# Performance work log

Hardware: AMD Instinct MI355X
Metric: run time of the kernel (lower is better)

Reference implementation:

```python
import jax, jax.numpy as jnp
import numpy as np

N_EMBD = 1024
N_HEAD = 16
HEAD_DIM = N_EMBD // N_HEAD
B, T = 4, 1024
EPS = 1e-5


def _linear_params(key, fan_in, fan_out):
    kw, kb = jax.random.split(key)
    bound = 1.0 / np.sqrt(fan_in)
    W = jax.random.uniform(kw, (fan_in, fan_out), minval=-bound, maxval=bound, dtype=jnp.float32)
    b = jax.random.uniform(kb, (fan_out,), minval=-bound, maxval=bound, dtype=jnp.float32)
    return W, b


def setup_inputs() -> dict:
    key = jax.random.key(0)
    ks = jax.random.split(key, 8)
    x = jax.random.normal(ks[0], (B, T, N_EMBD), dtype=jnp.float32)
    Wq, bq = _linear_params(ks[1], N_EMBD, N_EMBD)
    Wk, bk = _linear_params(ks[2], N_EMBD, N_EMBD)
    Wv, bv = _linear_params(ks[3], N_EMBD, N_EMBD)
    Wp, bp = _linear_params(ks[4], N_EMBD, N_EMBD)
    W1, b1 = _linear_params(ks[5], N_EMBD, 4 * N_EMBD)
    W2, b2 = _linear_params(ks[6], 4 * N_EMBD, N_EMBD)
    g1 = jnp.ones((N_EMBD,), jnp.float32); be1 = jnp.zeros((N_EMBD,), jnp.float32)
    g2 = jnp.ones((N_EMBD,), jnp.float32); be2 = jnp.zeros((N_EMBD,), jnp.float32)
    return {"x": x, "Wq": Wq, "bq": bq, "Wk": Wk, "bk": bk, "Wv": Wv, "bv": bv,
            "Wp": Wp, "bp": bp, "W1": W1, "b1": b1, "W2": W2, "b2": b2,
            "g1": g1, "be1": be1, "g2": g2, "be2": be2}


def _layernorm(x, g, b):
    mu = jnp.mean(x, axis=-1, keepdims=True)
    var = jnp.mean(jnp.square(x - mu), axis=-1, keepdims=True)
    return (x - mu) * jax.lax.rsqrt(var + EPS) * g + b


def _attention(x, Wq, bq, Wk, bk, Wv, bv, Wp, bp):
    Bsz, Tt, C = x.shape
    def heads(W, b):
        return (x @ W + b).reshape(Bsz, Tt, N_HEAD, HEAD_DIM).transpose(0, 2, 1, 3)  # [B,H,T,d]
    q, k, v = heads(Wq, bq), heads(Wk, bk), heads(Wv, bv)
    scores = jnp.einsum('bhqd,bhkd->bhqk', q, k) / np.sqrt(HEAD_DIM).astype(np.float32)
    causal = jnp.tril(jnp.ones((Tt, Tt), dtype=bool))
    scores = jnp.where(causal, scores, -jnp.inf)
    attn = jax.nn.softmax(scores, axis=-1)
    out = jnp.einsum('bhqk,bhkd->bhqd', attn, v)  # [B,H,T,d]
    out = out.transpose(0, 2, 1, 3).reshape(Bsz, Tt, C)
    return out @ Wp + bp


def _ff(x, W1, b1, W2, b2):
    h = jax.nn.gelu(x @ W1 + b1, approximate=False)  # torch nn.GELU default = exact erf
    return h @ W2 + b2


def reference(x, Wq, bq, Wk, bk, Wv, bv, Wp, bp, W1, b1, W2, b2, g1, be1, g2, be2):
    x = x + _attention(_layernorm(x, g1, be1), Wq, bq, Wk, bk, Wv, bv, Wp, bp)
    x = x + _ff(_layernorm(x, g2, be2), W1, b1, W2, b2)
    return x
```

## Files before the change

### kernel.cpp

```cpp
#include <hip/hip_runtime.h>
#include <hip/hip_bf16.h>

typedef __attribute__((ext_vector_type(8))) __bf16 bf16x8;
typedef __attribute__((ext_vector_type(4))) float f32x4;
typedef __attribute__((ext_vector_type(4))) unsigned short u16x4;
typedef unsigned short u16;

#define AS3(p) ((__attribute__((address_space(3))) void*)(p))
#define AS1(p) ((const __attribute__((address_space(1))) void*)(p))

__device__ __forceinline__ u16 f2b(float f) {
    __hip_bfloat16 h = __float2bfloat16(f);
    return __builtin_bit_cast(u16, h);
}

__device__ __forceinline__ float gelu_exact(float v) {
    const float z = v * 0.70710678118654752f;
    const float a = fabsf(z);
    const float t = __builtin_amdgcn_rcpf(1.0f + 0.3275911f * a);
    float p = 1.061405429f;
    p = p * t - 1.453152027f;
    p = p * t + 1.421413741f;
    p = p * t - 0.284496736f;
    p = p * t + 0.254829592f;
    p = p * t;
    float erfv = 1.0f - p * __expf(-a * a);
    erfv = copysignf(erfv, z);
    return 0.5f * v * (1.0f + erfv);
}

__global__ __launch_bounds__(256) void transpose_w(
    const float* __restrict__ W, u16* __restrict__ WT, int K, int N)
{
    __shared__ u16 tile[32][33];
    const int tx = threadIdx.x & 31, ty = threadIdx.x >> 5;
    const int n0 = blockIdx.x * 32, k0 = blockIdx.y * 32;
    #pragma unroll
    for (int p = 0; p < 4; ++p)
        tile[ty + p * 8][tx] = f2b(W[(size_t)(k0 + ty + p * 8) * N + n0 + tx]);
    __syncthreads();
    #pragma unroll
    for (int p = 0; p < 4; ++p)
        WT[(size_t)(n0 + ty + p * 8) * K + k0 + tx] = tile[tx][ty + p * 8];
}

__global__ __launch_bounds__(256) void transpose_w3(
    const float* __restrict__ W0, const float* __restrict__ W1,
    const float* __restrict__ W2, u16* __restrict__ WT)
{
    __shared__ u16 tile[32][33];
    const int z = blockIdx.z;
    const float* W = (z == 0) ? W0 : (z == 1) ? W1 : W2;
    u16* dst = WT + (size_t)z * 1024 * 1024;
    const int tx = threadIdx.x & 31, ty = threadIdx.x >> 5;
    const int n0 = blockIdx.x * 32, k0 = blockIdx.y * 32;
    #pragma unroll
    for (int p = 0; p < 4; ++p)
        tile[ty + p * 8][tx] = f2b(W[(size_t)(k0 + ty + p * 8) * 1024 + n0 + tx]);
    __syncthreads();
    #pragma unroll
    for (int p = 0; p < 4; ++p)
        dst[(size_t)(n0 + ty + p * 8) * 1024 + k0 + tx] = tile[tx][ty + p * 8];
}

__global__ __launch_bounds__(256) void ln_bf16(
    const float* __restrict__ xin, const float* __restrict__ gam,
    const float* __restrict__ bet, u16* __restrict__ yout)
{
    __shared__ float red[8];
    const int row = blockIdx.x, tid = threadIdx.x;
    float4 v = ((const float4*)(xin + (size_t)row * 1024))[tid];
    float s = v.x + v.y + v.z + v.w;
    #pragma unroll
    for (int o = 32; o > 0; o >>= 1) s += __shfl_xor(s, o, 64);
    if ((tid & 63) == 0) red[tid >> 6] = s;
    __syncthreads();
    const float mu = (red[0] + red[1] + red[2] + red[3]) * (1.f / 1024.f);
    const float dx = v.x - mu, dy = v.y - mu, dz = v.z - mu, dw = v.w - mu;
    float sq = dx * dx + dy * dy + dz * dz + dw * dw;
    #pragma unroll
    for (int o = 32; o > 0; o >>= 1) sq += __shfl_xor(sq, o, 64);
    if ((tid & 63) == 0) red[4 + (tid >> 6)] = sq;
    __syncthreads();
    const float var = (red[4] + red[5] + red[6] + red[7]) * (1.f / 1024.f);
    const float inv = rsqrtf(var + 1e-5f);
    const float4 G = ((const float4*)gam)[tid];
    const float4 Bt = ((const float4*)bet)[tid];
    u16x4 o;
    o[0] = f2b(dx * inv * G.x + Bt.x);
    o[1] = f2b(dy * inv * G.y + Bt.y);
    o[2] = f2b(dz * inv * G.z + Bt.z);
    o[3] = f2b(dw * inv * G.w + Bt.w);
    ((u16x4*)(yout + (size_t)row * 1024))[tid] = o;
}

__global__ __launch_bounds__(256) void reduce_ln(
    const float* __restrict__ p0, const float* __restrict__ p1,
    const float* __restrict__ bias, const float* __restrict__ resid,
    const float* __restrict__ gam, const float* __restrict__ bet,
    float* __restrict__ xout, u16* __restrict__ yout)
{
    __shared__ float red[8];
    const int row = blockIdx.x, tid = threadIdx.x;
    const size_t off = (size_t)row * 256 + tid;
    float4 a = ((const float4*)p0)[off];
    const float4 b = ((const float4*)p1)[off];
    const float4 r = ((const float4*)resid)[off];
    const float4 bs = ((const float4*)bias)[tid];
    a.x += b.x + r.x + bs.x; a.y += b.y + r.y + bs.y;
    a.z += b.z + r.z + bs.z; a.w += b.w + r.w + bs.w;
    ((float4*)xout)[off] = a;
    float s = a.x + a.y + a.z + a.w;
    #pragma unroll
    for (int o = 32; o > 0; o >>= 1) s += __shfl_xor(s, o, 64);
    if ((tid & 63) == 0) red[tid >> 6] = s;
    __syncthreads();
    const float mu = (red[0] + red[1] + red[2] + red[3]) * (1.f / 1024.f);
    const float dx = a.x - mu, dy = a.y - mu, dz = a.z - mu, dw = a.w - mu;
    float sq = dx * dx + dy * dy + dz * dz + dw * dw;
    #pragma unroll
    for (int o = 32; o > 0; o >>= 1) sq += __shfl_xor(sq, o, 64);
    if ((tid & 63) == 0) red[4 + (tid >> 6)] = sq;
    __syncthreads();
    const float var = (red[4] + red[5] + red[6] + red[7]) * (1.f / 1024.f);
    const float inv = rsqrtf(var + 1e-5f);
    const float4 G = ((const float4*)gam)[tid];
    const float4 Bt = ((const float4*)bet)[tid];
    u16x4 o;
    o[0] = f2b(dx * inv * G.x + Bt.x);
    o[1] = f2b(dy * inv * G.y + Bt.y);
    o[2] = f2b(dz * inv * G.z + Bt.z);
    o[3] = f2b(dw * inv * G.w + Bt.w);
    ((u16x4*)(yout + (size_t)row * 1024))[tid] = o;
}

__global__ __launch_bounds__(256) void reduce_add(
    const float* __restrict__ p0, const float* __restrict__ p1,
    const float* __restrict__ bias, const float* __restrict__ resid,
    float* __restrict__ out)
{
    const size_t i = (size_t)blockIdx.x * 256 + threadIdx.x;
    float4 a = ((const float4*)p0)[i];
    const float4 b = ((const float4*)p1)[i];
    const float4 r = ((const float4*)resid)[i];
    const float4 bs = ((const float4*)bias)[i & 255];
    a.x += b.x + r.x + bs.x; a.y += b.y + r.y + bs.y;
    a.z += b.z + r.z + bs.z; a.w += b.w + r.w + bs.w;
    ((float4*)out)[i] = a;
}

template <int MODE, int BM, int SK>
__global__ __launch_bounds__(256, (BM == 128 ? 3 : 2)) void gemm_bf16(
    const u16* __restrict__ A, const u16* __restrict__ BT,
    const float* __restrict__ b0, const float* __restrict__ b1,
    const float* __restrict__ b2,
    void* __restrict__ outp, int M, int N, int K)
{
    constexpr int WM = BM / 2;
    constexpr int MI = WM / 16;
    constexpr int NI = 4;
    constexpr int AJ = BM / 64;
    constexpr int AELEM = BM * 32;
    constexpr int BELEM = 128 * 32;
    __shared__ u16 Asm[3 * AELEM];
    __shared__ u16 Bsm[3 * BELEM];

    const int tid = threadIdx.x;
    const int lane = tid & 63, wid = tid >> 6;
    const int wm = wid >> 1, wn = wid & 1;
    const int g = lane >> 4, l16 = lane & 15;
    const int sx = (l16 >> 1) & 3;
    const int sslot = (lane & 3) ^ ((lane >> 3) & 3);

    const int nBN = N >> 7;
    const int per = (M / BM) * nBN;
    const int cpx = gridDim.x >> 3;
    const int wg = (blockIdx.x & 7) * cpx + (blockIdx.x >> 3);
    const int skid = (SK > 1) ? (wg / per) : 0;
    const int rem = wg - skid * per;
    const int bm0 = (rem / nBN) * BM, bn0 = (rem % nBN) * 128;
    const int kb = skid * (K / SK);

    f32x4 acc[MI][NI] = {};

    const u16* aBase = A + (size_t)(bm0 + (lane >> 2)) * K + kb + sslot * 8;
    const u16* bBase = BT + (size_t)(bn0 + (lane >> 2)) * K + kb + sslot * 8;

    auto stage = [&](int kt, int buf) {
        u16* adst = Asm + buf * AELEM + lane * 8;
        u16* bdst = Bsm + buf * BELEM + lane * 8;
        #pragma unroll
        for (int j = 0; j < AJ; ++j) {
            const int ia = wid * AJ + j;
            __builtin_amdgcn_global_load_lds(AS1(aBase + (size_t)(ia * 16) * K + kt),
                                             AS3(adst + ia * 512), 16, 0, 0);
        }
        #pragma unroll
        for (int j = 0; j < 2; ++j) {
            const int ib = wid * 2 + j;
            __builtin_amdgcn_global_load_lds(AS1(bBase + (size_t)(ib * 16) * K + kt),
                                             AS3(bdst + ib * 512), 16, 0, 0);
        }
    };

    const int nt = K / (32 * SK);
    stage(0, 0);
    stage(32, 1);
    int cur = 0, pre = 2;

    for (int t = 0; t < nt; ++t) {
        if (t + 1 < nt) {
            if constexpr (BM == 256) asm volatile("s_waitcnt vmcnt(6)" ::: "memory");
            else                     asm volatile("s_waitcnt vmcnt(4)" ::: "memory");
        } else {
            asm volatile("s_waitcnt vmcnt(0)" ::: "memory");
        }
        __builtin_amdgcn_s_barrier();
        __builtin_amdgcn_sched_barrier(0);

        const u16* asrc = Asm + cur * AELEM;
        const u16* bsrc = Bsm + cur * BELEM;
        bf16x8 af[MI], bfr[NI];
        #pragma unroll
        for (int mi = 0; mi < MI; ++mi) {
            const int r = wm * WM + mi * 16 + l16;
            af[mi] = *(const bf16x8*)(asrc + r * 32 + ((g ^ sx) << 3));
        }
        #pragma unroll
        for (int ni = 0; ni < NI; ++ni) {
            const int c = wn * 64 + ni * 16 + l16;
            bfr[ni] = *(const bf16x8*)(bsrc + c * 32 + ((g ^ sx) << 3));
        }
        if (t + 2 < nt) stage((t + 2) * 32, pre);

        #pragma unroll
        for (int mi = 0; mi < MI; ++mi)
            #pragma unroll
            for (int ni = 0; ni < NI; ++ni)
                acc[mi][ni] = __builtin_amdgcn_mfma_f32_16x16x32_bf16(
                    af[mi], bfr[ni], acc[mi][ni], 0, 0, 0);

        pre = cur;
        cur = (cur == 2) ? 0 : cur + 1;
    }

    #pragma unroll
    for (int mi = 0; mi < MI; ++mi) {
        #pragma unroll
        for (int ni = 0; ni < NI; ++ni) {
            #pragma unroll
            for (int j = 0; j < 4; ++j) {
                const int m = bm0 + wm * WM + mi * 16 + g * 4 + j;
                const int n = bn0 + wn * 64 + ni * 16 + l16;
                float v = acc[mi][ni][j];
                if constexpr (MODE == 0) {
                    const float bias = (n < 1024) ? b0[n]
                                      : (n < 2048) ? b1[n - 1024] : b2[n - 2048];
                    ((u16*)outp)[(size_t)m * N + n] = f2b(v + bias);
                } else if constexpr (MODE == 2) {
                    ((u16*)outp)[(size_t)m * N + n] = f2b(gelu_exact(v + b0[n]));
                } else {
                    float* pout = (float*)outp + (size_t)skid * M * N;
                    pout[(size_t)m * N + n] = v;
                }
            }
        }
    }
}

__global__ __launch_bounds__(256) void attn_fwd(
    const u16* __restrict__ qkv, u16* __restrict__ outp)
{
    __shared__ u16 Ksm[64 * 72];
    __shared__ u16 Vsm[64 * 72];
    __shared__ u16 Psm[4][16 * 72];
    const int tid = threadIdx.x, lane = tid & 63, w = tid >> 6;
    const int lin = blockIdx.y * 8 + blockIdx.x;
    const int xq = (lin >> 3) & 7;
    const int bh = (((lin >> 6) & 7) << 3) | (lin & 7);
    const int b = bh >> 4, h = bh & 15;
    const int g = lane >> 4, l16 = lane & 15;
    const int skv = tid >> 4;
    const int sd4 = (tid & 15) * 4;

    const u16* kvb = qkv + (size_t)(b * 1024) * 3072 + 1024 + h * 64;

    u16x4 kreg[4], vreg[4];
    auto issue = [&](int kv0) {
        const u16* kb = kvb + (size_t)kv0 * 3072;
        #pragma unroll
        for (int i = 0; i < 4; ++i)
            kreg[i] = *(const u16x4*)(kb + (size_t)(skv + 16 * i) * 3072 + sd4);
        #pragma unroll
        for (int i = 0; i < 4; ++i)
            vreg[i] = *(const u16x4*)(kb + (size_t)(4 * skv + i) * 3072 + 1024 + sd4);
    };

    #pragma unroll
    for (int half = 0; half < 2; ++half) {
        const int qt = half ? (15 - xq) : xq;
        const int q0 = qt * 64;

        bf16x8 qf0, qf1;
        {
            const u16* qp = qkv + (size_t)(b * 1024 + q0 + w * 16 + l16) * 3072
                            + h * 64 + g * 8;
            qf0 = *(const bf16x8*)qp;
            qf1 = *(const bf16x8*)(qp + 32);
        }
        float m_run[4] = {-1e30f, -1e30f, -1e30f, -1e30f};
        float l_run[4] = {0.f, 0.f, 0.f, 0.f};
        f32x4 oacc[4] = {};

        issue(0);

        for (int kvt = 0; kvt <= qt; ++kvt) {
            const int kv0 = kvt * 64;
            __syncthreads();
            #pragma unroll
            for (int i = 0; i < 4; ++i)
                *(u16x4*)(Ksm + (skv + 16 * i) * 72 + sd4) = kreg[i];
            #pragma unroll
            for (int j = 0; j < 4; ++j) {
                u16x4 t;
                t[0] = vreg[0][j]; t[1] = vreg[1][j];
                t[2] = vreg[2][j]; t[3] = vreg[3][j];
                *(u16x4*)(Vsm + (sd4 + j) * 72 + 4 * skv) = t;
            }
            __syncthreads();
            if (kvt < qt) issue(kv0 + 64);

            f32x4 s[4];
            #pragma unroll
            for (int t = 0; t < 4; ++t) {
                const bf16x8 kf0 = *(const bf16x8*)(Ksm + (t * 16 + l16) * 72 + g * 8);
                const bf16x8 kf1 = *(const bf16x8*)(Ksm + (t * 16 + l16) * 72 + 32 + g * 8);
                f32x4 z = {};
                z = __builtin_amdgcn_mfma_f32_16x16x32_bf16(qf0, kf0, z, 0, 0, 0);
                z = __builtin_amdgcn_mfma_f32_16x16x32_bf16(qf1, kf1, z, 0, 0, 0);
                s[t] = z;
            }
            float mx[4] = {-1e30f, -1e30f, -1e30f, -1e30f};
            #pragma unroll
            for (int t = 0; t < 4; ++t)
                #pragma unroll
                for (int j = 0; j < 4; ++j) {
                    const int qrow = q0 + w * 16 + g * 4 + j;
                    const int kvc = kv0 + t * 16 + l16;
                    float v = s[t][j] * 0.125f;
                    if (kvc > qrow) v = -1e30f;
                    s[t][j] = v;
                    mx[j] = fmaxf(mx[j], v);
                }
            #pragma unroll
            for (int o = 1; o < 16; o <<= 1)
                #pragma unroll
                for (int j = 0; j < 4; ++j)
                    mx[j] = fmaxf(mx[j], __shfl_xor(mx[j], o, 16));
            float alpha[4], rs[4];
            #pragma unroll
            for (int j = 0; j < 4; ++j) {
                const float mn = fmaxf(m_run[j], mx[j]);
                alpha[j] = __expf(m_run[j] - mn);
                m_run[j] = mn;
                rs[j] = 0.f;
            }
            #pragma unroll
            for (int t = 0; t < 4; ++t)
                #pragma unroll
                for (int j = 0; j < 4; ++j) {
                    const float p = __expf(s[t][j] - m_run[j]);
                    s[t][j] = p;
                    rs[j] += p;
                }
            #pragma unroll
            for (int o = 1; o < 16; o <<= 1)
                #pragma unroll
                for (int j = 0; j < 4; ++j)
                    rs[j] += __shfl_xor(rs[j], o, 16);
            #pragma unroll
            for (int j = 0; j < 4; ++j)
                l_run[j] = l_run[j] * alpha[j] + rs[j];
            #pragma unroll
            for (int dt = 0; dt < 4; ++dt)
                #pragma unroll
                for (int j = 0; j < 4; ++j)
                    oacc[dt][j] *= alpha[j];
            #pragma unroll
            for (int t = 0; t < 4; ++t)
                #pragma unroll
                for (int j = 0; j < 4; ++j)
                    Psm[w][(g * 4 + j) * 72 + t * 16 + l16] = f2b(s[t][j]);
            const bf16x8 pf0 = *(const bf16x8*)(&Psm[w][l16 * 72 + g * 8]);
            const bf16x8 pf1 = *(const bf16x8*)(&Psm[w][l16 * 72 + 32 + g * 8]);
            #pragma unroll
            for (int dt = 0; dt < 4; ++dt) {
                const bf16x8 vf0 = *(const bf16x8*)(Vsm + (dt * 16 + l16) * 72 + g * 8);
                const bf16x8 vf1 = *(const bf16x8*)(Vsm + (dt * 16 + l16) * 72 + 32 + g * 8);
                oacc[dt] = __builtin_amdgcn_mfma_f32_16x16x32_bf16(pf0, vf0, oacc[dt], 0, 0, 0);
                oacc[dt] = __builtin_amdgcn_mfma_f32_16x16x32_bf16(pf1, vf1, oacc[dt], 0, 0, 0);
            }
        }
        #pragma unroll
        for (int dt = 0; dt < 4; ++dt)
            #pragma unroll
            for (int j = 0; j < 4; ++j) {
                const int m = b * 1024 + q0 + w * 16 + g * 4 + j;
                const int col = h * 64 + dt * 16 + l16;
                outp[(size_t)m * 1024 + col] = f2b(oacc[dt][j] / l_run[j]);
            }
    }
}

extern "C" void kernel_launch(void* const* d_in, const int* in_sizes, int n_in,
                              void* d_out, int out_size, void* d_ws, size_t ws_size,
                              hipStream_t stream)
{
    const float* x   = (const float*)d_in[0];
    const float* Wq  = (const float*)d_in[1];
    const float* bq  = (const float*)d_in[2];
    const float* Wk  = (const float*)d_in[3];
    const float* bk  = (const float*)d_in[4];
    const float* Wv  = (const float*)d_in[5];
    const float* bv  = (const float*)d_in[6];
    const float* Wp  = (const float*)d_in[7];
    const float* bp  = (const float*)d_in[8];
    const float* W1  = (const float*)d_in[9];
    const float* b1  = (const float*)d_in[10];
    const float* W2  = (const float*)d_in[11];
    const float* b2  = (const float*)d_in[12];
    const float* g1  = (const float*)d_in[13];
    const float* be1 = (const float*)d_in[14];
    const float* g2  = (const float*)d_in[15];
    const float* be2 = (const float*)d_in[16];

    char* ws = (char*)d_ws;
    const size_t MB = 1024 * 1024;
    u16*   ln_buf = (u16*)(ws);
    u16*   qkv    = (u16*)(ws + 8 * MB);
    u16*   attn_o = (u16*)(ws + 32 * MB);
    float* x1     = (float*)(ws + 40 * MB);
    u16*   hbuf   = (u16*)(ws + 56 * MB);
    u16*   wqkvT  = (u16*)(ws + 88 * MB);
    u16*   wpT    = (u16*)(ws + 94 * MB);
    u16*   w1T    = (u16*)(ws + 96 * MB);
    u16*   w2T    = (u16*)(ws + 104 * MB);
    float* projP  = (float*)(ws + 56 * MB);
    float* ff2P   = (float*)(ws + 8 * MB);

    transpose_w3<<<dim3(32, 32, 3), 256, 0, stream>>>(Wq, Wk, Wv, wqkvT);
    transpose_w<<<dim3(32, 32), 256, 0, stream>>>(Wp, wpT, 1024, 1024);
    transpose_w<<<dim3(128, 32), 256, 0, stream>>>(W1, w1T, 1024, 4096);
    transpose_w<<<dim3(32, 128), 256, 0, stream>>>(W2, w2T, 4096, 1024);

    ln_bf16<<<4096, 256, 0, stream>>>(x, g1, be1, ln_buf);
    gemm_bf16<0, 128, 1><<<768, 256, 0, stream>>>(
        ln_buf, wqkvT, bq, bk, bv, qkv, 4096, 3072, 1024);
    attn_fwd<<<dim3(8, 64), 256, 0, stream>>>(qkv, attn_o);
    gemm_bf16<3, 128, 2><<<512, 256, 0, stream>>>(
        attn_o, wpT, nullptr, nullptr, nullptr, projP, 4096, 1024, 1024);
    reduce_ln<<<4096, 256, 0, stream>>>(
        projP, projP + 4096 * 1024, bp, x, g2, be2, x1, ln_buf);
    gemm_bf16<2, 256, 1><<<512, 256, 0, stream>>>(
        ln_buf, w1T, b1, nullptr, nullptr, hbuf, 4096, 4096, 1024);
    gemm_bf16<3, 128, 2><<<512, 256, 0, stream>>>(
        hbuf, w2T, nullptr, nullptr, nullptr, ff2P, 4096, 1024, 4096);
    reduce_add<<<4096, 256, 0, stream>>>(
        ff2P, ff2P + 4096 * 1024, b2, x1, (float*)d_out);
}
```

Baseline: 221.4 us.

## Double-buffer attention K/V in LDS with XOR swizzle, prescaled Q and exp2

Restructures the flash-attention kernel so K/V tiles are double-buffered in shared memory, with one barrier per iteration instead of two. Padded shared-memory rows are replaced by an XOR swizzle. Q is prescaled by log2(e)/sqrt(d) in the QKV GEMM epilogue so the softmax can use exp2 directly. The causal mask is applied only on the diagonal tile, row sums come from an MFMA against a vector of ones instead of shuffle reductions, and the final divide becomes a reciprocal multiply. The MFMA row sum is computed from bf16-rounded probabilities, which slightly changes numerics, and the doubled shared-memory use may lower occupancy.

```diff
diff --git a/kernel.cpp b/kernel.cpp
--- a/kernel.cpp
+++ b/kernel.cpp
@@ -8,6 +8,8 @@
 
 #define AS3(p) ((__attribute__((address_space(3))) void*)(p))
 #define AS1(p) ((const __attribute__((address_space(1))) void*)(p))
+
+#define QSCALE 0.18033688011112042f
 
 __device__ __forceinline__ u16 f2b(float f) {
     __hip_bfloat16 h = __float2bfloat16(f);
@@ -256,7 +258,9 @@
                 if constexpr (MODE == 0) {
                     const float bias = (n < 1024) ? b0[n]
                                       : (n < 2048) ? b1[n - 1024] : b2[n - 2048];
-                    ((u16*)outp)[(size_t)m * N + n] = f2b(v + bias);
+                    float o = v + bias;
+                    if (n < 1024) o *= QSCALE;
+                    ((u16*)outp)[(size_t)m * N + n] = f2b(o);
                 } else if constexpr (MODE == 2) {
                     ((u16*)outp)[(size_t)m * N + n] = f2b(gelu_exact(v + b0[n]));
                 } else {
@@ -271,9 +275,9 @@
 __global__ __launch_bounds__(256) void attn_fwd(
     const u16* __restrict__ qkv, u16* __restrict__ outp)
 {
-    __shared__ u16 Ksm[64 * 72];
-    __shared__ u16 Vsm[64 * 72];
-    __shared__ u16 Psm[4][16 * 72];
+    __shared__ u16 Ksm[2][64 * 64];
+    __shared__ u16 Vsm[2][64 * 64];
+    __shared__ u16 Psm[4][16 * 64];
     const int tid = threadIdx.x, lane = tid & 63, w = tid >> 6;
     const int lin = blockIdx.y * 8 + blockIdx.x;
     const int xq = (lin >> 3) & 7;
@@ -285,6 +289,10 @@
 
     const u16* kvb = qkv + (size_t)(b * 1024) * 3072 + 1024 + h * 64;
 
+    bf16x8 vones;
+    #pragma unroll
+    for (int e = 0; e < 8; ++e) vones[e] = __builtin_bit_cast(__bf16, (u16)0x3F80);
+
     u16x4 kreg[4], vreg[4];
     auto issue = [&](int kv0) {
         const u16* kb = kvb + (size_t)kv0 * 3072;
@@ -294,6 +302,21 @@
         #pragma unroll
         for (int i = 0; i < 4; ++i)
             vreg[i] = *(const u16x4*)(kb + (size_t)(4 * skv + i) * 3072 + 1024 + sd4);
+    };
+    auto stage_lds = [&](int buf) {
+        #pragma unroll
+        for (int i = 0; i < 4; ++i) {
+            const int row = skv + 16 * i;
+            *(u16x4*)(&Ksm[buf][row * 64 + (sd4 ^ ((row & 7) << 3))]) = kreg[i];
+        }
+        #pragma unroll
+        for (int j = 0; j < 4; ++j) {
+            u16x4 t;
+            t[0] = vreg[0][j]; t[1] = vreg[1][j];
+            t[2] = vreg[2][j]; t[3] = vreg[3][j];
+            const int row = sd4 + j;
+            *(u16x4*)(&Vsm[buf][row * 64 + ((4 * skv) ^ ((row & 7) << 3))]) = t;
+        }
     };
 
     #pragma unroll
@@ -313,101 +336,104 @@
         f32x4 oacc[4] = {};
 
         issue(0);
+        __syncthreads();
+        stage_lds(0);
+        if (qt > 0) issue(64);
+        __syncthreads();
+        int cur = 0;
 
         for (int kvt = 0; kvt <= qt; ++kvt) {
-            const int kv0 = kvt * 64;
-            __syncthreads();
-            #pragma unroll
-            for (int i = 0; i < 4; ++i)
-                *(u16x4*)(Ksm + (skv + 16 * i) * 72 + sd4) = kreg[i];
-            #pragma unroll
-            for (int j = 0; j < 4; ++j) {
-                u16x4 t;
-                t[0] = vreg[0][j]; t[1] = vreg[1][j];
-                t[2] = vreg[2][j]; t[3] = vreg[3][j];
-                *(u16x4*)(Vsm + (sd4 + j) * 72 + 4 * skv) = t;
-            }
-            __syncthreads();
-            if (kvt < qt) issue(kv0 + 64);
-
             f32x4 s[4];
             #pragma unroll
             for (int t = 0; t < 4; ++t) {
-                const bf16x8 kf0 = *(const bf16x8*)(Ksm + (t * 16 + l16) * 72 + g * 8);
-                const bf16x8 kf1 = *(const bf16x8*)(Ksm + (t * 16 + l16) * 72 + 32 + g * 8);
+                const int r = t * 16 + l16;
+                const int sw = (r & 7) << 3;
+                const bf16x8 kf0 = *(const bf16x8*)(&Ksm[cur][r * 64 + ((g * 8) ^ sw)]);
+                const bf16x8 kf1 = *(const bf16x8*)(&Ksm[cur][r * 64 + (((g + 4) * 8) ^ sw)]);
                 f32x4 z = {};
                 z = __builtin_amdgcn_mfma_f32_16x16x32_bf16(qf0, kf0, z, 0, 0, 0);
                 z = __builtin_amdgcn_mfma_f32_16x16x32_bf16(qf1, kf1, z, 0, 0, 0);
                 s[t] = z;
             }
+            if (kvt == qt) {
+                #pragma unroll
+                for (int t = 0; t < 4; ++t)
+                    #pragma unroll
+                    for (int j = 0; j < 4; ++j) {
+                        const int qrow = q0 + w * 16 + g * 4 + j;
+                        const int kvc = q0 + t * 16 + l16;
+                        if (kvc > qrow) s[t][j] = -1e30f;
+                    }
+            }
             float mx[4] = {-1e30f, -1e30f, -1e30f, -1e30f};
             #pragma unroll
             for (int t = 0; t < 4; ++t)
                 #pragma unroll
-                for (int j = 0; j < 4; ++j) {
-                    const int qrow = q0 + w * 16 + g * 4 + j;
-                    const int kvc = kv0 + t * 16 + l16;
-                    float v = s[t][j] * 0.125f;
-                    if (kvc > qrow) v = -1e30f;
-                    s[t][j] = v;
-                    mx[j] = fmaxf(mx[j], v);
-                }
+                for (int j = 0; j < 4; ++j)
+                    mx[j] = fmaxf(mx[j], s[t][j]);
             #pragma unroll
             for (int o = 1; o < 16; o <<= 1)
                 #pragma unroll
                 for (int j = 0; j < 4; ++j)
                     mx[j] = fmaxf(mx[j], __shfl_xor(mx[j], o, 16));
-            float alpha[4], rs[4];
+            float alpha[4];
             #pragma unroll
             for (int j = 0; j < 4; ++j) {
                 const float mn = fmaxf(m_run[j], mx[j]);
-                alpha[j] = __expf(m_run[j] - mn);
+                alpha[j] = __builtin_amdgcn_exp2f(m_run[j] - mn);
                 m_run[j] = mn;
-                rs[j] = 0.f;
             }
             #pragma unroll
             for (int t = 0; t < 4; ++t)
                 #pragma unroll
+                for (int j = 0; j < 4; ++j)
+                    s[t][j] = __builtin_amdgcn_exp2f(s[t][j] - m_run[j]);
+            #pragma unroll
+            for (int t = 0; t < 4; ++t)
+                #pragma unroll
                 for (int j = 0; j < 4; ++j) {
-                    const float p = __expf(s[t][j] - m_run[j]);
-                    s[t][j] = p;
-                    rs[j] += p;
+                    const int row = g * 4 + j;
+                    Psm[w][row * 64 + ((t * 16 + l16) ^ ((row & 7) << 3))] = f2b(s[t][j]);
                 }
-            #pragma unroll
-            for (int o = 1; o < 16; o <<= 1)
-                #pragma unroll
-                for (int j = 0; j < 4; ++j)
-                    rs[j] += __shfl_xor(rs[j], o, 16);
+            const int psw = (l16 & 7) << 3;
+            const bf16x8 pf0 = *(const bf16x8*)(&Psm[w][l16 * 64 + ((g * 8) ^ psw)]);
+            const bf16x8 pf1 = *(const bf16x8*)(&Psm[w][l16 * 64 + (((g + 4) * 8) ^ psw)]);
+            f32x4 sum = {};
+            sum = __builtin_amdgcn_mfma_f32_16x16x32_bf16(pf0, vones, sum, 0, 0, 0);
+            sum = __builtin_amdgcn_mfma_f32_16x16x32_bf16(pf1, vones, sum, 0, 0, 0);
             #pragma unroll
             for (int j = 0; j < 4; ++j)
-                l_run[j] = l_run[j] * alpha[j] + rs[j];
+                l_run[j] = l_run[j] * alpha[j] + sum[j];
             #pragma unroll
             for (int dt = 0; dt < 4; ++dt)
                 #pragma unroll
                 for (int j = 0; j < 4; ++j)
                     oacc[dt][j] *= alpha[j];
             #pragma unroll
-            for (int t = 0; t < 4; ++t)
-                #pragma unroll
-                for (int j = 0; j < 4; ++j)
-                    Psm[w][(g * 4 + j) * 72 + t * 16 + l16] = f2b(s[t][j]);
-            const bf16x8 pf0 = *(const bf16x8*)(&Psm[w][l16 * 72 + g * 8]);
-            const bf16x8 pf1 = *(const bf16x8*)(&Psm[w][l16 * 72 + 32 + g * 8]);
-            #pragma unroll
             for (int dt = 0; dt < 4; ++dt) {
-                const bf16x8 vf0 = *(const bf16x8*)(Vsm + (dt * 16 + l16) * 72 + g * 8);
-                const bf16x8 vf1 = *(const bf16x8*)(Vsm + (dt * 16 + l16) * 72 + 32 + g * 8);
+                const int rv = dt * 16 + l16;
+                const int sw = (rv & 7) << 3;
+                const bf16x8 vf0 = *(const bf16x8*)(&Vsm[cur][rv * 64 + ((g * 8) ^ sw)]);
+                const bf16x8 vf1 = *(const bf16x8*)(&Vsm[cur][rv * 64 + (((g + 4) * 8) ^ sw)]);
                 oacc[dt] = __builtin_amdgcn_mfma_f32_16x16x32_bf16(pf0, vf0, oacc[dt], 0, 0, 0);
                 oacc[dt] = __builtin_amdgcn_mfma_f32_16x16x32_bf16(pf1, vf1, oacc[dt], 0, 0, 0);
             }
-        }
+            if (kvt < qt) {
+                stage_lds(cur ^ 1);
+                if (kvt + 2 <= qt) issue((kvt + 2) * 64);
+                __syncthreads();
+                cur ^= 1;
+            }
+        }
+        #pragma unroll
+        for (int j = 0; j < 4; ++j) l_run[j] = __builtin_amdgcn_rcpf(l_run[j]);
         #pragma unroll
         for (int dt = 0; dt < 4; ++dt)
             #pragma unroll
             for (int j = 0; j < 4; ++j) {
                 const int m = b * 1024 + q0 + w * 16 + g * 4 + j;
                 const int col = h * 64 + dt * 16 + l16;
-                outp[(size_t)m * 1024 + col] = f2b(oacc[dt][j] / l_run[j]);
+                outp[(size_t)m * 1024 + col] = f2b(oacc[dt][j] * l_run[j]);
             }
     }
 }
```

Result: faster. 212.3 us (-4.1%).
